# Kernel tuning notes

Hardware: AMD Instinct MI355X
Metric: run time of the kernel (lower is better)

The kernel has to match this reference:

```python
import jax, jax.numpy as jnp
import numpy as np

N_CLUSTERS = 64
COLLAPSE_REG = 0.1
H_SMOOTH = -0.0001
H_ALPHA = 0.0001
H_LAMBDA = 0.0001


def setup_inputs() -> dict:
    key = jax.random.key(0)
    ks = jax.random.split(key, 6)
    n, d, k = 65536, 512, N_CLUSTERS
    e0 = 1048576  # directed edges before symmetrization
    features = jax.random.normal(ks[0], (n, d), jnp.float32)
    s = jax.random.randint(ks[1], (e0,), 0, n)
    t = jax.random.randint(ks[2], (e0,), 0, n)
    v = jax.random.uniform(ks[3], (e0,), jnp.float32)
    # symmetrize adjacency (real graph datasets are undirected -> L = D - A is PSD)
    edge_src = jnp.concatenate([s, t]).astype(jnp.int64)
    edge_dst = jnp.concatenate([t, s]).astype(jnp.int64)
    edge_vals = jnp.concatenate([v, v])
    W = jax.random.normal(ks[4], (d, k), jnp.float32) / np.sqrt(d).astype(np.float32)
    b = jnp.zeros((k,), jnp.float32)
    return dict(features=features, edge_src=edge_src, edge_dst=edge_dst,
                edge_vals=edge_vals, W=W, b=b)


def reference(features, edge_src, edge_dst, edge_vals, W, b):
    n, d = features.shape
    k = W.shape[1]
    # assignments = softmax(Dense(features))
    S = jax.nn.softmax(features @ W + b, axis=1)  # [n,k]
    cluster_sizes = jnp.sum(S, axis=0)            # [k]
    S_pool = S / cluster_sizes                    # [n,k]
    # sparse column-degree (tf.sparse.reduce_sum axis=0) and edge count
    deg_col = jax.ops.segment_sum(edge_vals, edge_dst, num_segments=n)[:, None]  # [n,1]
    m = jnp.sum(deg_col)
    # A @ S via edge-list gather/scatter (sparse_dense_matmul)
    AS = jax.ops.segment_sum(edge_vals[:, None] * S[edge_dst], edge_src,
                             num_segments=n)      # [n,k]
    graph_pooled = AS.T @ S                       # S^T A S, [k,k]
    normalizer = ((S.T @ deg_col) @ (deg_col.T @ S)) / 2.0 / m  # [k,k]
    spectral_loss = -jnp.trace(graph_pooled - normalizer) / 2.0 / m
    collapse_loss = (jnp.linalg.norm(cluster_sizes) / n
                     * jnp.sqrt(jnp.float32(k)) - 1.0)
    # pooled features
    FP = jax.nn.selu(S_pool.T @ features)         # [k,d]
    # FGC loss chain: Laplacian L = D_row - A applied sparsely
    deg_row = jax.ops.segment_sum(edge_vals, edge_src, num_segments=n)[:, None]
    LS = deg_row * S - AS                         # L @ S, [n,k]
    StLS = LS.T @ S                               # smoothness1 = S^T L S, [k,k]
    # log(det(StLS + ones)) computed stably via slogdet (det is positive: PSD + rank-1)
    _sign, logabsdet = jnp.linalg.slogdet(StLS + jnp.ones_like(StLS))
    smoothness_loss = logabsdet * H_SMOOTH
    # trace((L S) @ FP @ FP^T): trace of [n,k] matrix = sum of first k diagonal entries
    trace_loss = jnp.einsum('ic,cd,id->', LS[:k], FP, FP)
    frob_loss = jnp.linalg.norm(S @ FP - features) * H_ALPHA
    one_two_loss = jnp.linalg.norm(jnp.sum(jnp.abs(S), axis=0)) * H_LAMBDA
    fgc_loss = smoothness_loss + trace_loss + frob_loss + one_two_loss
    total_loss = spectral_loss + COLLAPSE_REG * collapse_loss + fgc_loss
    return FP, S, total_loss
```

## Files before the change

kernel.cpp:

```cpp
#include <hip/hip_runtime.h>
#include <hip/hip_bf16.h>
#include <cstdint>
#include <cstddef>

typedef unsigned short u16;
typedef float f32x4 __attribute__((ext_vector_type(4)));
typedef short bf16x8 __attribute__((ext_vector_type(8)));
typedef unsigned short u16x8 __attribute__((ext_vector_type(8)));

__device__ __forceinline__ u16 f2bf(float f) {
    uint32_t u = __float_as_uint(f);
    u += 0x7fffu + ((u >> 16) & 1u);
    return (u16)(u >> 16);
}
__device__ __forceinline__ float bf2f(u16 h) {
    return __uint_as_float(((uint32_t)h) << 16);
}

#define SWZ(c) ((((c) ^ ((c) >> 3)) & 7) << 2)
#define SWZ2(c) ((((c) >> 2) & 7) << 2)

__device__ __forceinline__ void softbar() {
    asm volatile("s_waitcnt lgkmcnt(0)" ::: "memory");
    __builtin_amdgcn_s_barrier();
    __builtin_amdgcn_sched_barrier(0);
}

__global__ __launch_bounds__(256) void k_prep(const float* __restrict__ Wg, u16* __restrict__ Wt) {
    int idx = blockIdx.x * 256 + threadIdx.x;
    int k = idx >> 6, c = idx & 63;
    int lin = c * 512 + (k ^ ((c & 7) << 3));
    Wt[lin] = f2bf(Wg[idx]);
}

__global__ __launch_bounds__(256) void k1(const float* __restrict__ F,
    const u16* __restrict__ WtG, const float* __restrict__ bias,
    float* __restrict__ S_out, u16* __restrict__ Sbf,
    float* __restrict__ sizes, float* __restrict__ scal) {
    __shared__ __align__(16) u16 Wl2[2][4096];
    __shared__ __align__(16) u16 Al[2][4096];
    __shared__ float red4[4];
    const int tid = threadIdx.x;
    const int row0 = blockIdx.x * 64;

    const int lane = tid & 63;
    const int wv = __builtin_amdgcn_readfirstlane(tid >> 6);
    const int l15 = lane & 15, lq = lane >> 4;
    f32x4 acc[4];
    #pragma unroll
    for (int tn = 0; tn < 4; tn++)
        #pragma unroll
        for (int e = 0; e < 4; e++) acc[tn][e] = 0.f;
    float sumf2 = 0.f;
    const int sr = tid >> 2, skq = tid & 3;
    const int sw = (sr & 7) << 3;

    int buf = 0;
    for (int k0 = 0; k0 < 512; k0 += 64) {
        const float* fp = F + (size_t)(row0 + sr) * 512 + k0 + skq * 16;
        float4 v[4];
        u16 h[16];
        #pragma unroll
        for (int q = 0; q < 4; q++) v[q] = ((const float4*)fp)[q];
        #pragma unroll
        for (int q = 0; q < 4; q++) {
            sumf2 += v[q].x * v[q].x + v[q].y * v[q].y + v[q].z * v[q].z + v[q].w * v[q].w;
            h[q * 4 + 0] = f2bf(v[q].x); h[q * 4 + 1] = f2bf(v[q].y);
            h[q * 4 + 2] = f2bf(v[q].z); h[q * 4 + 3] = f2bf(v[q].w);
        }
        #pragma unroll
        for (int half = 0; half < 2; half++) {
            u16x8 pk;
            #pragma unroll
            for (int e2 = 0; e2 < 8; e2++) pk[e2] = h[half * 8 + e2];
            *(u16x8*)&Al[buf][sr * 64 + ((skq * 16 + half * 8) ^ sw)] = pk;
        }
        #pragma unroll
        for (int j = tid; j < 512; j += 256) {
            const int c = j >> 3, q = j & 7;
            ((uint4*)&Wl2[buf][c * 64])[q] = ((const uint4*)(WtG + c * 512 + k0))[q];
        }
        __syncthreads();
        #pragma unroll
        for (int kk = 0; kk < 64; kk += 32) {
            const int arow = wv * 16 + l15;
            bf16x8 a = *(const bf16x8*)&Al[buf][arow * 64 + ((kk + lq * 8) ^ ((arow & 7) << 3))];
            #pragma unroll
            for (int tn = 0; tn < 4; tn++) {
                const int bc = tn * 16 + l15;
                bf16x8 b = *(const bf16x8*)&Wl2[buf][bc * 64 + ((kk + lq * 8) ^ ((bc & 7) << 3))];
                acc[tn] = __builtin_amdgcn_mfma_f32_16x16x32_bf16(a, b, acc[tn], 0, 0, 0);
            }
        }
        buf ^= 1;
    }

    float bias4[4], szacc[4] = {0.f, 0.f, 0.f, 0.f};
    #pragma unroll
    for (int tn = 0; tn < 4; tn++) bias4[tn] = bias[tn * 16 + l15];
    #pragma unroll
    for (int r2 = 0; r2 < 4; r2++) {
        float L[4];
        #pragma unroll
        for (int tn = 0; tn < 4; tn++) L[tn] = acc[tn][r2] + bias4[tn];
        float mx = fmaxf(fmaxf(L[0], L[1]), fmaxf(L[2], L[3]));
        #pragma unroll
        for (int mm = 1; mm < 16; mm <<= 1) mx = fmaxf(mx, __shfl_xor(mx, mm));
        float e[4], s = 0.f;
        #pragma unroll
        for (int tn = 0; tn < 4; tn++) { e[tn] = __expf(L[tn] - mx); s += e[tn]; }
        #pragma unroll
        for (int mm = 1; mm < 16; mm <<= 1) s += __shfl_xor(s, mm);
        const float inv = 1.f / s;
        const size_t grow = (size_t)(row0 + wv * 16 + lq * 4 + r2);
        #pragma unroll
        for (int tn = 0; tn < 4; tn++) {
            const float svl = e[tn] * inv;
            S_out[grow * 64 + tn * 16 + l15] = svl;
            Sbf[grow * 64 + tn * 16 + l15] = f2bf(svl);
            szacc[tn] += svl;
        }
    }
    #pragma unroll
    for (int tn = 0; tn < 4; tn++) {
        float vs = szacc[tn];
        vs += __shfl_xor(vs, 16);
        vs += __shfl_xor(vs, 32);
        if (lq == 0) atomicAdd(sizes + tn * 16 + l15, vs);
    }
    #pragma unroll
    for (int mm = 1; mm < 64; mm <<= 1) sumf2 += __shfl_xor(sumf2, mm);
    if (lane == 0) red4[wv] = sumf2;
    __syncthreads();
    if (tid == 0) atomicAdd(scal + 1, red4[0] + red4[1] + red4[2] + red4[3]);
}

__global__ __launch_bounds__(512) void k_mid(const int* __restrict__ esrc,
    const int* __restrict__ edst, const float* __restrict__ ev,
    const u16* __restrict__ Sbf, const float* __restrict__ S,
    const float* __restrict__ F, const int E2,
    float* __restrict__ GP8, float* __restrict__ SDS8, float* __restrict__ uv8,
    float* __restrict__ AS64, float* __restrict__ deg64, float* __restrict__ scal,
    float* __restrict__ G) {
    __shared__ uint32_t Tl[2][2048];
    __shared__ uint32_t Pl[2][2048];
    __shared__ uint32_t Ql[2][2048];
    __shared__ uint32_t Rl[2][2048];
    __shared__ uint32_t Ss2[2048];
    __shared__ uint32_t Fs2[4096];
    const int tid = threadIdx.x;
    const int lane = tid & 63;
    const int wv8 = __builtin_amdgcn_readfirstlane(tid >> 6);
    const int wv = wv8;
    const int l15 = lane & 15, lq = lane >> 4;
    const int xcd = blockIdx.x & 7;
    float* __restrict__ GPmy = GP8 + (size_t)xcd * 4096;
    float* __restrict__ SDSmy = SDS8 + (size_t)xcd * 4096;
    float* __restrict__ umy = uv8 + (size_t)xcd * 64;

    const bool isP = tid < 256;
    const int st = tid & 255;
    const int p = st >> 3, g = st & 7;
    float vsum = 0.f;
    float uacc[8];
    #pragma unroll
    for (int j = 0; j < 8; j++) uacc[j] = 0.f;
    f32x4 aG[2], aSd[2];
    #pragma unroll
    for (int t = 0; t < 2; t++)
        #pragma unroll
        for (int r = 0; r < 4; r++) { aG[t][r] = 0.f; aSd[t][r] = 0.f; }
    const int ma = 16 * (wv & 3) + l15;
    const int aoff = ma * 32, aswz = SWZ(ma);
    const int nb0r = 32 * (wv >> 2) + l15;
    const int nb1r = nb0r + 16;
    const int b0off = nb0r * 32, b0swz = SWZ(nb0r);
    const int b1off = nb1r * 32, b1swz = SWZ(nb1r);

    const int d0 = (blockIdx.x & 3) * 128;
    const int kblk = blockIdx.x >> 2;
    const int cwv = wv8 & 3, dh = wv8 >> 2;
    f32x4 acc2[4];
    #pragma unroll
    for (int t8 = 0; t8 < 4; t8++)
        #pragma unroll
        for (int r = 0; r < 4; r++) acc2[t8][r] = 0.f;
    const int s_ip = tid >> 3;
    const int s_cs = (tid & 7) * 8;
    const int tF = tid - 256;
    const int f_dg = tF & 31;
    const int f_ipb = tF >> 5;

    const int nch = E2 >> 6;
    const int stride = gridDim.x;
    int ch = blockIdx.x;
    const int sweep_left = (ch < nch) ? ((nch - ch + stride - 1) / stride) : 0;

    int2 ia_c, ib_c, ia_n, ib_n;
    float2 vv_c, vv_n;
    {
        const int e0 = (ch << 6) + 2 * p;
        ia_c = isP ? *(const int2*)&edst[e0] : *(const int2*)&esrc[e0];
        ib_c = isP ? *(const int2*)&esrc[e0] : *(const int2*)&edst[e0];
        vv_c = *(const float2*)&ev[e0];
    }
    u16x8 ra_c = *(const u16x8*)&Sbf[(size_t)ia_c.x * 64 + 8 * g];
    u16x8 rb_c = *(const u16x8*)&Sbf[(size_t)ia_c.y * 64 + 8 * g];
    int chn = ch + stride;
    {
        const int chc = chn < nch ? chn : (nch - 1);
        const int e0 = (chc << 6) + 2 * p;
        ia_n = isP ? *(const int2*)&edst[e0] : *(const int2*)&esrc[e0];
        ib_n = isP ? *(const int2*)&esrc[e0] : *(const int2*)&edst[e0];
        vv_n = *(const float2*)&ev[e0];
    }

    int buf = 0;
    int sw_done = 0, mm_done = 0;
    const int total = sweep_left + 8;
    for (int step = 0; step < total; step++) {
        const bool do_mm = (mm_done < 8) &&
                           ((sw_done >= (mm_done + 1) * 4) || (sw_done == sweep_left));
        if (do_mm) {
            const int i0 = kblk * 512 + mm_done * 64;
            if (isP) {
                const u16x8 r0 = *(const u16x8*)&Sbf[(size_t)(i0 + 2 * s_ip) * 64 + s_cs];
                const u16x8 r1 = *(const u16x8*)&Sbf[(size_t)(i0 + 2 * s_ip + 1) * 64 + s_cs];
                #pragma unroll
                for (int j = 0; j < 8; j++) {
                    const int c = s_cs + j;
                    Ss2[c * 32 + (s_ip ^ SWZ2(c))] =
                        (uint32_t)(u16)r0[j] | ((uint32_t)(u16)r1[j] << 16);
                }
            } else {
                #pragma unroll
                for (int s = 0; s < 4; s++) {
                    const int ip = f_ipb + 8 * s;
                    const float4 a = *(const float4*)(F + (size_t)(i0 + 2 * ip) * 512 + d0 + 4 * f_dg);
                    const float4 b = *(const float4*)(F + (size_t)(i0 + 2 * ip + 1) * 512 + d0 + 4 * f_dg);
                    const float al[4] = {a.x, a.y, a.z, a.w};
                    const float bl[4] = {b.x, b.y, b.z, b.w};
                    #pragma unroll
                    for (int j = 0; j < 4; j++) {
                        const int d = 4 * f_dg + j;
                        Fs2[d * 32 + (ip ^ SWZ2(d))] =
                            (uint32_t)f2bf(al[j]) | ((uint32_t)f2bf(bl[j]) << 16);
                    }
                }
            }
            softbar();
            #pragma unroll
            for (int kk = 0; kk < 64; kk += 32) {
                const int w0 = (kk >> 1) + (lq << 2);
                const int ca = 16 * cwv + l15;
                const bf16x8 afrag = *(const bf16x8*)&Ss2[ca * 32 + (w0 ^ SWZ2(ca))];
                #pragma unroll
                for (int t8r = 0; t8r < 4; t8r++) {
                    const int d = 16 * (4 * dh + t8r) + l15;
                    const bf16x8 bfrag = *(const bf16x8*)&Fs2[d * 32 + (w0 ^ SWZ2(d))];
                    acc2[t8r] = __builtin_amdgcn_mfma_f32_16x16x32_bf16(afrag, bfrag, acc2[t8r], 0, 0, 0);
                }
            }
            softbar();
            mm_done++;
        } else {
            if (isP) {
                #pragma unroll
                for (int j = 0; j < 8; j++) {
                    const int c = 8 * g + j;
                    const int off = c * 32 + (p ^ SWZ(c));
                    Tl[buf][off] = (uint32_t)(u16)ra_c[j] | ((uint32_t)(u16)rb_c[j] << 16);
                    Pl[buf][off] = (uint32_t)f2bf(vv_c.x * bf2f((u16)ra_c[j])) |
                                   ((uint32_t)f2bf(vv_c.y * bf2f((u16)rb_c[j])) << 16);
                }
            } else {
                #pragma unroll
                for (int j = 0; j < 8; j++) {
                    const int c = 8 * g + j;
                    const int off = c * 32 + (p ^ SWZ(c));
                    Ql[buf][off] = (uint32_t)(u16)ra_c[j] | ((uint32_t)(u16)rb_c[j] << 16);
                    Rl[buf][off] = (uint32_t)f2bf(vv_c.x * bf2f((u16)ra_c[j])) |
                                   ((uint32_t)f2bf(vv_c.y * bf2f((u16)rb_c[j])) << 16);
                }
            }
            #pragma unroll
            for (int j = 0; j < 8; j++)
                uacc[j] = fmaf(vv_c.x, bf2f((u16)ra_c[j]),
                          fmaf(vv_c.y, bf2f((u16)rb_c[j]), uacc[j]));
            if (!isP && g == 0) vsum += vv_c.x + vv_c.y;
            if (g == 0) {
                if (ib_c.x < 64) atomicAdd(deg64 + ib_c.x, vv_c.x);
                if (ib_c.y < 64) atomicAdd(deg64 + ib_c.y, vv_c.y);
            }
            if (ib_c.x < 64) {
                const float4 fa = *(const float4*)(S + (size_t)ia_c.x * 64 + 8 * g);
                const float4 fb = *(const float4*)(S + (size_t)ia_c.x * 64 + 8 * g + 4);
                float* dst = AS64 + ib_c.x * 64 + 8 * g;
                atomicAdd(dst + 0, vv_c.x * fa.x); atomicAdd(dst + 1, vv_c.x * fa.y);
                atomicAdd(dst + 2, vv_c.x * fa.z); atomicAdd(dst + 3, vv_c.x * fa.w);
                atomicAdd(dst + 4, vv_c.x * fb.x); atomicAdd(dst + 5, vv_c.x * fb.y);
                atomicAdd(dst + 6, vv_c.x * fb.z); atomicAdd(dst + 7, vv_c.x * fb.w);
            }
            if (ib_c.y < 64) {
                const float4 fa = *(const float4*)(S + (size_t)ia_c.y * 64 + 8 * g);
                const float4 fb = *(const float4*)(S + (size_t)ia_c.y * 64 + 8 * g + 4);
                float* dst = AS64 + ib_c.y * 64 + 8 * g;
                atomicAdd(dst + 0, vv_c.y * fa.x); atomicAdd(dst + 1, vv_c.y * fa.y);
                atomicAdd(dst + 2, vv_c.y * fa.z); atomicAdd(dst + 3, vv_c.y * fa.w);
                atomicAdd(dst + 4, vv_c.y * fb.x); atomicAdd(dst + 5, vv_c.y * fb.y);
                atomicAdd(dst + 6, vv_c.y * fb.z); atomicAdd(dst + 7, vv_c.y * fb.w);
            }
            const u16x8 ra_n = *(const u16x8*)&Sbf[(size_t)ia_n.x * 64 + 8 * g];
            const u16x8 rb_n = *(const u16x8*)&Sbf[(size_t)ia_n.y * 64 + 8 * g];
            const int chnn = chn + stride;
            int2 ia_nn, ib_nn;
            float2 vv_nn;
            {
                const int chc = chnn < nch ? chnn : (nch - 1);
                const int e0 = (chc << 6) + 2 * p;
                ia_nn = isP ? *(const int2*)&edst[e0] : *(const int2*)&esrc[e0];
                ib_nn = isP ? *(const int2*)&esrc[e0] : *(const int2*)&edst[e0];
                vv_nn = *(const float2*)&ev[e0];
            }
            softbar();
            #pragma unroll
            for (int half = 0; half < 2; half++) {
                const int w0 = half * 16 + lq * 4;
                const bf16x8 afP = *(const bf16x8*)&Pl[buf][aoff + (w0 ^ aswz)];
                const bf16x8 afR = *(const bf16x8*)&Rl[buf][aoff + (w0 ^ aswz)];
                const bf16x8 qb0 = *(const bf16x8*)&Ql[buf][b0off + (w0 ^ b0swz)];
                const bf16x8 qb1 = *(const bf16x8*)&Ql[buf][b1off + (w0 ^ b1swz)];
                const bf16x8 tb0 = *(const bf16x8*)&Tl[buf][b0off + (w0 ^ b0swz)];
                const bf16x8 tb1 = *(const bf16x8*)&Tl[buf][b1off + (w0 ^ b1swz)];
                aG[0] = __builtin_amdgcn_mfma_f32_16x16x32_bf16(afP, qb0, aG[0], 0, 0, 0);
                aG[1] = __builtin_amdgcn_mfma_f32_16x16x32_bf16(afP, qb1, aG[1], 0, 0, 0);
                aSd[0] = __builtin_amdgcn_mfma_f32_16x16x32_bf16(afR, qb0, aSd[0], 0, 0, 0);
                aSd[1] = __builtin_amdgcn_mfma_f32_16x16x32_bf16(afR, qb1, aSd[1], 0, 0, 0);
                aSd[0] = __builtin_amdgcn_mfma_f32_16x16x32_bf16(afP, tb0, aSd[0], 0, 0, 0);
                aSd[1] = __builtin_amdgcn_mfma_f32_16x16x32_bf16(afP, tb1, aSd[1], 0, 0, 0);
            }
            ch = chn;
            ia_c = ia_n; ib_c = ib_n; vv_c = vv_n; ra_c = ra_n; rb_c = rb_n;
            ia_n = ia_nn; ib_n = ib_nn; vv_n = vv_nn;
            chn = chnn;
            buf ^= 1;
            sw_done++;
        }
    }
    #pragma unroll
    for (int t = 0; t < 2; t++)
        #pragma unroll
        for (int r = 0; r < 4; r++) {
            const int c1 = 16 * (wv & 3) + 4 * lq + r;
            const int c2 = 32 * (wv >> 2) + 16 * t + l15;
            atomicAdd(GPmy + c1 * 64 + c2, aG[t][r]);
            atomicAdd(SDSmy + c1 * 64 + c2, aSd[t][r]);
        }
    #pragma unroll
    for (int j = 0; j < 8; j++) {
        uacc[j] += __shfl_xor(uacc[j], 8);
        uacc[j] += __shfl_xor(uacc[j], 16);
        uacc[j] += __shfl_xor(uacc[j], 32);
    }
    if (lane < 8) {
        #pragma unroll
        for (int j = 0; j < 8; j++)
            atomicAdd(umy + 8 * lane + j, uacc[j]);
    }
    if (wv >= 4) {
        #pragma unroll
        for (int mm = 1; mm < 64; mm <<= 1) vsum += __shfl_xor(vsum, mm);
        if (lane == 0) atomicAdd(scal + 0, vsum + vsum);
    }
    #pragma unroll
    for (int t8r = 0; t8r < 4; t8r++)
        #pragma unroll
        for (int r = 0; r < 4; r++) {
            const int c = 16 * cwv + 4 * lq + r;
            const int d = d0 + 16 * (4 * dh + t8r) + l15;
            atomicAdd(G + (size_t)c * 512 + d, acc2[t8r][r]);
        }
}

__global__ __launch_bounds__(256) void k_mrg(const float* __restrict__ GP8,
    const float* __restrict__ SDS8, const float* __restrict__ uv8,
    float* __restrict__ GP, float* __restrict__ SDS, float* __restrict__ u_vec) {
    const int bid = blockIdx.x;
    const int t = threadIdx.x;
    if (bid < 16) {
        const int j = bid * 256 + t;
        const int jt = (j & 63) * 64 + (j >> 6);
        float s = 0.f;
        #pragma unroll
        for (int c = 0; c < 8; c++)
            s += GP8[(size_t)c * 4096 + j] + GP8[(size_t)c * 4096 + jt];
        GP[j] = s;
    } else if (bid < 32) {
        const int j = (bid - 16) * 256 + t;
        float s = 0.f;
        #pragma unroll
        for (int c = 0; c < 8; c++) s += SDS8[(size_t)c * 4096 + j];
        SDS[j] = s;
    } else if (t < 64) {
        float s = 0.f;
        #pragma unroll
        for (int c = 0; c < 8; c++) s += uv8[c * 64 + t];
        u_vec[t] = s;
    }
}

__global__ __launch_bounds__(256) void k_kk(const u16* __restrict__ Sbf,
    float* __restrict__ SS) {
    __shared__ float Pss[4][16][64];
    const int tid = threadIdx.x, lane = tid & 63;
    const int wv = __builtin_amdgcn_readfirstlane(tid >> 6);
    const int cs = blockIdx.x & 3, c0 = cs * 16;
    const int rbase = (blockIdx.x >> 2) * 512 + wv * 128;
    float ss[16];
    #pragma unroll
    for (int cc = 0; cc < 16; cc++) ss[cc] = 0.f;
    for (int r = 0; r < 128; r++) {
        const int i = rbase + r;
        const float sv = bf2f(Sbf[(size_t)i * 64 + lane]);
        const u16* srow = Sbf + (size_t)i * 64 + c0;
        #pragma unroll
        for (int cc = 0; cc < 16; cc++)
            ss[cc] = fmaf(bf2f(srow[cc]), sv, ss[cc]);
    }
    #pragma unroll
    for (int cc = 0; cc < 16; cc++) Pss[wv][cc][lane] = ss[cc];
    __syncthreads();
    for (int q = 0; q < 4; q++) {
        const int cell = tid * 4 + q, cc = cell >> 6, l = cell & 63;
        atomicAdd(SS + (c0 + cc) * 64 + l,
                  Pss[0][cc][l] + Pss[1][cc][l] + Pss[2][cc][l] + Pss[3][cc][l]);
    }
}

__device__ __forceinline__ float bred256(float v, float* red) {
    #pragma unroll
    for (int mm = 1; mm < 64; mm <<= 1) v += __shfl_xor(v, mm);
    const int t = threadIdx.x;
    __syncthreads();
    if ((t & 63) == 0) red[t >> 6] = v;
    __syncthreads();
    return red[0] + red[1] + red[2] + red[3];
}

__global__ __launch_bounds__(256) void k_fp(const float* __restrict__ G,
    const float* __restrict__ sizes, float* __restrict__ FP, float* __restrict__ scal) {
    __shared__ float red[4];
    const int idx = blockIdx.x * 256 + threadIdx.x;
    const int c = idx >> 9;
    const float g = G[idx];
    const float x = g / sizes[c];
    const float fp = 1.0507009873554805f * (x > 0.f ? x : 1.6732632423543772f * (__expf(x) - 1.f));
    FP[idx] = fp;
    const float gd = bred256(g * fp, red);
    if (threadIdx.x == 0) atomicAdd(scal + 2, gd);
}

__global__ __launch_bounds__(256) void k_fft(const float* __restrict__ FP, float* __restrict__ FFt) {
    __shared__ float red[256];
    const int c = blockIdx.x;
    const int cp = threadIdx.x & 63, part = threadIdx.x >> 6;
    float a = 0.f;
    const int dbase = part * 128;
    for (int dd = 0; dd < 128; dd++)
        a = fmaf(FP[c * 512 + dbase + dd], FP[cp * 512 + dbase + dd], a);
    red[threadIdx.x] = a;
    __syncthreads();
    if (threadIdx.x < 64)
        FFt[c * 64 + threadIdx.x] = red[threadIdx.x] + red[threadIdx.x + 64] +
                                    red[threadIdx.x + 128] + red[threadIdx.x + 192];
}

__global__ __launch_bounds__(256) void k_lu(const float* __restrict__ SDS,
    const float* __restrict__ GP, float* __restrict__ scal) {
    __shared__ float M[64][65];
    __shared__ float red[4];
    const int tid = threadIdx.x;
    const int l = tid & 63, q = tid >> 6;
    #pragma unroll
    for (int j = 0; j < 16; j++) {
        const int c = q * 16 + j;
        M[l][c] = SDS[l * 64 + c] - GP[l * 64 + c] + 1.0f;
    }
    __syncthreads();
    for (int k = 0; k < 63; k++) {
        if (l > k) {
            const float f = M[l][k] / M[k][k];
            const int cend = q * 16 + 16;
            for (int c = (q * 16 > k + 1 ? q * 16 : k + 1); c < cend; c++)
                M[l][c] = fmaf(-f, M[k][c], M[l][c]);
        }
        __syncthreads();
    }
    float v = (tid < 64) ? logf(fabsf(M[tid][tid])) : 0.f;
    const float ld = bred256(v, red);
    if (tid == 0) scal[3] = ld;
}

__global__ __launch_bounds__(256) void k_final(const float* __restrict__ GP,
    const float* __restrict__ SS, const float* __restrict__ FFt, const float* __restrict__ u_vec,
    const float* __restrict__ sizes, const float* __restrict__ deg64,
    const float* __restrict__ AS64, const float* __restrict__ S,
    const float* __restrict__ scal, float* __restrict__ out_loss, const float fn) {
    __shared__ float red[4];
    const int t = threadIdx.x;
    float sA = 0.f, trl = 0.f, trg = 0.f, u2 = 0.f, sz2 = 0.f;
    for (int q = t; q < 4096; q += 256) sA += SS[q] * FFt[q];
    for (int q = t; q < 4096; q += 256) {
        const int i = q >> 6, c = q & 63;
        const float ls = deg64[i] * S[i * 64 + c] - AS64[q];
        trl += ls * FFt[c * 64 + i];
    }
    if (t < 64) { trg = GP[t * 65]; u2 = u_vec[t] * u_vec[t]; sz2 = sizes[t] * sizes[t]; }
    sA = bred256(sA, red);
    trl = bred256(trl, red);
    trg = bred256(trg, red);
    u2 = bred256(u2, red);
    sz2 = bred256(sz2, red);
    if (t == 0) {
        const float m = scal[0], sumF2 = scal[1], gfp = scal[2], lad = scal[3];
        const float spectral = -(trg - u2 / (2.f * m)) / (2.f * m);
        const float collapse = sqrtf(sz2) / fn * 8.f - 1.f;
        const float frob = sqrtf(fmaxf(sA - 2.f * gfp + sumF2, 0.f)) * 1e-4f;
        const float one_two = sqrtf(sz2) * 1e-4f;
        const float smooth = lad * (-1e-4f);
        out_loss[0] = spectral + 0.1f * collapse + smooth + trl + frob + one_two;
    }
}

extern "C" void kernel_launch(void* const* d_in, const int* in_sizes, int n_in,
                              void* d_out, int out_size, void* d_ws, size_t ws_size,
                              hipStream_t stream) {
    const float* F = (const float*)d_in[0];
    const int* esrc = (const int*)d_in[1];
    const int* edst = (const int*)d_in[2];
    const float* ev = (const float*)d_in[3];
    const float* Wg = (const float*)d_in[4];
    const float* bg = (const float*)d_in[5];
    const int n = in_sizes[0] / 512;
    const int E = in_sizes[1];
    const int E2 = E >> 1;

    float* outF = (float*)d_out;
    float* outS = outF + 64 * 512;
    float* outL = outS + (size_t)n * 64;

    char* w = (char*)d_ws;
    float* sizes = (float*)w;
    float* u_vec = sizes + 64;
    float* scal = u_vec + 64;
    float* G = scal + 64;
    float* SS = G + 64 * 512;
    float* AS64 = SS + 4096;
    float* deg64 = AS64 + 4096;
    float* GP8 = deg64 + 64;
    float* SDS8 = GP8 + 8 * 4096;
    float* u8buf = SDS8 + 8 * 4096;
    char* zend = (char*)(u8buf + 512);
    const size_t zero_bytes = (size_t)(zend - w);
    float* GP = (float*)zend;
    float* SDS = GP + 4096;
    float* FFt = SDS + 4096;
    u16* Sbf = (u16*)(FFt + 4096);
    u16* Wt = Sbf + (size_t)n * 64;

    hipMemsetAsync(d_ws, 0, zero_bytes, stream);
    k_prep<<<128, 256, 0, stream>>>(Wg, Wt);
    k1<<<n / 64, 256, 0, stream>>>(F, Wt, bg, outS, Sbf, sizes, scal);
    k_mid<<<512, 512, 0, stream>>>(esrc, edst, ev, Sbf, outS, F, E2,
                                   GP8, SDS8, u8buf, AS64, deg64, scal, G);
    k_mrg<<<33, 256, 0, stream>>>(GP8, SDS8, u8buf, GP, SDS, u_vec);
    k_kk<<<(n / 512) * 4, 256, 0, stream>>>(Sbf, SS);
    k_fp<<<128, 256, 0, stream>>>(G, sizes, outF, scal);
    k_fft<<<64, 256, 0, stream>>>(outF, FFt);
    k_lu<<<1, 256, 0, stream>>>(SDS, GP, scal);
    k_final<<<1, 256, 0, stream>>>(GP, SS, FFt, u_vec, sizes, deg64, AS64, outS, scal, outL, (float)n);
}
```

Before: 475.9 us.

## Preload full W into LDS in k1; build edge-scaled MFMA operands on the fly in k_mid

In k1, the whole transposed bf16 W (64x512) is loaded into shared memory once per block, and the per-k-step W tile copy and double buffering are removed. A second barrier is added after each k-step so the single A buffer can be reused safely. In k_mid, the Pl/Rl LDS arrays holding edge-value-scaled S rows are dropped. The scaled A fragments are now recomputed in registers from Tl/Ql plus a small per-edge value array, which cuts LDS writes and footprint but adds ALU conversion work per MFMA step and an extra sync per k-step in k1.

```diff
diff --git a/kernel.cpp b/kernel.cpp
--- a/kernel.cpp
+++ b/kernel.cpp
@@ -37,11 +37,13 @@
     const u16* __restrict__ WtG, const float* __restrict__ bias,
     float* __restrict__ S_out, u16* __restrict__ Sbf,
     float* __restrict__ sizes, float* __restrict__ scal) {
-    __shared__ __align__(16) u16 Wl2[2][4096];
-    __shared__ __align__(16) u16 Al[2][4096];
+    __shared__ __align__(16) u16 Wl[64 * 512];
+    __shared__ __align__(16) u16 Al[64 * 64];
     __shared__ float red4[4];
     const int tid = threadIdx.x;
     const int row0 = blockIdx.x * 64;
+    for (int j = tid; j < 4096; j += 256)
+        ((uint4*)Wl)[j] = ((const uint4*)WtG)[j];
 
     const int lane = tid & 63;
     const int wv = __builtin_amdgcn_readfirstlane(tid >> 6);
@@ -55,7 +57,6 @@
     const int sr = tid >> 2, skq = tid & 3;
     const int sw = (sr & 7) << 3;
 
-    int buf = 0;
     for (int k0 = 0; k0 < 512; k0 += 64) {
         const float* fp = F + (size_t)(row0 + sr) * 512 + k0 + skq * 16;
         float4 v[4];
@@ -73,26 +74,21 @@
             u16x8 pk;
             #pragma unroll
             for (int e2 = 0; e2 < 8; e2++) pk[e2] = h[half * 8 + e2];
-            *(u16x8*)&Al[buf][sr * 64 + ((skq * 16 + half * 8) ^ sw)] = pk;
-        }
-        #pragma unroll
-        for (int j = tid; j < 512; j += 256) {
-            const int c = j >> 3, q = j & 7;
-            ((uint4*)&Wl2[buf][c * 64])[q] = ((const uint4*)(WtG + c * 512 + k0))[q];
+            *(u16x8*)&Al[sr * 64 + ((skq * 16 + half * 8) ^ sw)] = pk;
         }
         __syncthreads();
         #pragma unroll
         for (int kk = 0; kk < 64; kk += 32) {
             const int arow = wv * 16 + l15;
-            bf16x8 a = *(const bf16x8*)&Al[buf][arow * 64 + ((kk + lq * 8) ^ ((arow & 7) << 3))];
+            bf16x8 a = *(const bf16x8*)&Al[arow * 64 + ((kk + lq * 8) ^ ((arow & 7) << 3))];
             #pragma unroll
             for (int tn = 0; tn < 4; tn++) {
                 const int bc = tn * 16 + l15;
-                bf16x8 b = *(const bf16x8*)&Wl2[buf][bc * 64 + ((kk + lq * 8) ^ ((bc & 7) << 3))];
+                bf16x8 b = *(const bf16x8*)&Wl[bc * 512 + ((k0 + kk + lq * 8) ^ ((bc & 7) << 3))];
                 acc[tn] = __builtin_amdgcn_mfma_f32_16x16x32_bf16(a, b, acc[tn], 0, 0, 0);
             }
         }
-        buf ^= 1;
+        __syncthreads();
     }
 
     float bias4[4], szacc[4] = {0.f, 0.f, 0.f, 0.f};
@@ -143,9 +139,8 @@
     float* __restrict__ AS64, float* __restrict__ deg64, float* __restrict__ scal,
     float* __restrict__ G) {
     __shared__ uint32_t Tl[2][2048];
-    __shared__ uint32_t Pl[2][2048];
     __shared__ uint32_t Ql[2][2048];
-    __shared__ uint32_t Rl[2][2048];
+    __shared__ __align__(8) float2 Vt[2][32];
     __shared__ uint32_t Ss2[2048];
     __shared__ uint32_t Fs2[4096];
     const int tid = threadIdx.x;
@@ -268,19 +263,16 @@
                 #pragma unroll
                 for (int j = 0; j < 8; j++) {
                     const int c = 8 * g + j;
-                    const int off = c * 32 + (p ^ SWZ(c));
-                    Tl[buf][off] = (uint32_t)(u16)ra_c[j] | ((uint32_t)(u16)rb_c[j] << 16);
-                    Pl[buf][off] = (uint32_t)f2bf(vv_c.x * bf2f((u16)ra_c[j])) |
-                                   ((uint32_t)f2bf(vv_c.y * bf2f((u16)rb_c[j])) << 16);
+                    Tl[buf][c * 32 + (p ^ SWZ(c))] =
+                        (uint32_t)(u16)ra_c[j] | ((uint32_t)(u16)rb_c[j] << 16);
                 }
+                if (g == 0) Vt[buf][p] = vv_c;
             } else {
                 #pragma unroll
                 for (int j = 0; j < 8; j++) {
                     const int c = 8 * g + j;
-                    const int off = c * 32 + (p ^ SWZ(c));
-                    Ql[buf][off] = (uint32_t)(u16)ra_c[j] | ((uint32_t)(u16)rb_c[j] << 16);
-                    Rl[buf][off] = (uint32_t)f2bf(vv_c.x * bf2f((u16)ra_c[j])) |
-                                   ((uint32_t)f2bf(vv_c.y * bf2f((u16)rb_c[j])) << 16);
+                    Ql[buf][c * 32 + (p ^ SWZ(c))] =
+                        (uint32_t)(u16)ra_c[j] | ((uint32_t)(u16)rb_c[j] << 16);
                 }
             }
             #pragma unroll
@@ -326,8 +318,17 @@
             #pragma unroll
             for (int half = 0; half < 2; half++) {
                 const int w0 = half * 16 + lq * 4;
-                const bf16x8 afP = *(const bf16x8*)&Pl[buf][aoff + (w0 ^ aswz)];
-                const bf16x8 afR = *(const bf16x8*)&Rl[buf][aoff + (w0 ^ aswz)];
+                const bf16x8 tA = *(const bf16x8*)&Tl[buf][aoff + (w0 ^ aswz)];
+                const bf16x8 qA = *(const bf16x8*)&Ql[buf][aoff + (w0 ^ aswz)];
+                bf16x8 afP, afR;
+                #pragma unroll
+                for (int i = 0; i < 4; i++) {
+                    const float2 vv = Vt[buf][w0 + i];
+                    afP[2 * i]     = (short)f2bf(vv.x * bf2f((u16)tA[2 * i]));
+                    afP[2 * i + 1] = (short)f2bf(vv.y * bf2f((u16)tA[2 * i + 1]));
+                    afR[2 * i]     = (short)f2bf(vv.x * bf2f((u16)qA[2 * i]));
+                    afR[2 * i + 1] = (short)f2bf(vv.y * bf2f((u16)qA[2 * i + 1]));
+                }
                 const bf16x8 qb0 = *(const bf16x8*)&Ql[buf][b0off + (w0 ^ b0swz)];
                 const bf16x8 qb1 = *(const bf16x8*)&Ql[buf][b1off + (w0 ^ b1swz)];
                 const bf16x8 tb0 = *(const bf16x8*)&Tl[buf][b0off + (w0 ^ b0swz)];
```

Result: no change. 481.1 us (+1.1%).
